# Performance work log

Hardware: AMD Instinct MI355X
Metric: run time of the kernel (lower is better)

## Reference

```python
import jax, jax.numpy as jnp
import numpy as np

L, C, H = 12, 1024, 16  # n_layer, n_embd, n_head
D = C // H
EPS = 1e-5

def gelu_new(x):
    # GPT-2 tanh-approximate GELU
    return 0.5 * x * (1.0 + jnp.tanh(np.sqrt(2.0 / np.pi).astype(np.float32) * (x + 0.044715 * x ** 3)))

def layernorm(x, g, b):
    mu = jnp.mean(x, axis=-1, keepdims=True)
    var = jnp.mean(jnp.square(x - mu), axis=-1, keepdims=True)
    return (x - mu) * jax.lax.rsqrt(var + EPS) * g + b

def setup_inputs() -> dict:
    key = jax.random.key(0)
    ks = jax.random.split(key, 8)
    std = 0.02
    inp = {
        'inputs_embeds': jax.random.normal(ks[0], (1, 1024, C), jnp.float32),
        'attention_mask': jnp.ones((1, 1024), jnp.float32),
        'ln1_g': jnp.ones((L, C), jnp.float32), 'ln1_b': jnp.zeros((L, C), jnp.float32),
        'Wqkv': jax.random.normal(ks[1], (L, C, 3 * C), jnp.float32) * std,
        'bqkv': jnp.zeros((L, 3 * C), jnp.float32),
        'Wo': jax.random.normal(ks[2], (L, C, C), jnp.float32) * (std / np.sqrt(2 * L)),
        'bo': jnp.zeros((L, C), jnp.float32),
        'ln2_g': jnp.ones((L, C), jnp.float32), 'ln2_b': jnp.zeros((L, C), jnp.float32),
        'Wfc': jax.random.normal(ks[3], (L, C, 4 * C), jnp.float32) * std,
        'bfc': jnp.zeros((L, 4 * C), jnp.float32),
        'Wmp': jax.random.normal(ks[4], (L, 4 * C, C), jnp.float32) * (std / np.sqrt(2 * L)),
        'bmp': jnp.zeros((L, C), jnp.float32),
        'lnf_g': jnp.ones((C,), jnp.float32), 'lnf_b': jnp.zeros((C,), jnp.float32),
    }
    return inp

def reference(inputs_embeds, attention_mask, ln1_g, ln1_b, Wqkv, bqkv, Wo, bo,
              ln2_g, ln2_b, Wfc, bfc, Wmp, bmp, lnf_g, lnf_b):
    B, T, _ = inputs_embeds.shape
    # padding mask -> additive bias [B,1,1,T] (broadcasts over heads and query dim)
    mask_add = -1e9 * (1.0 - attention_mask)[:, None, None, :]
    scale = 1.0 / np.sqrt(D).astype(np.float32)

    def block(x, p):
        g1, b1, Wq, bq, Wo_, bo_, g2, b2, Wf, bf, Wm, bm = p
        h = layernorm(x, g1, b1)
        qkv = h @ Wq + bq                                  # [B,T,3C]
        q, k, v = jnp.split(qkv, 3, axis=-1)
        q = q.reshape(B, T, H, D).transpose(0, 2, 1, 3)    # [B,H,T,D]
        k = k.reshape(B, T, H, D).transpose(0, 2, 1, 3)
        v = v.reshape(B, T, H, D).transpose(0, 2, 1, 3)
        att = jnp.einsum('bhqd,bhkd->bhqk', q, k) * scale + mask_add
        att = jax.nn.softmax(att, axis=-1)
        y = jnp.einsum('bhqk,bhkd->bhqd', att, v)
        y = y.transpose(0, 2, 1, 3).reshape(B, T, C)
        x = x + (y @ Wo_ + bo_)
        h2 = layernorm(x, g2, b2)
        x = x + (gelu_new(h2 @ Wf + bf) @ Wm + bm)
        return x, None

    params = (ln1_g, ln1_b, Wqkv, bqkv, Wo, bo, ln2_g, ln2_b, Wfc, bfc, Wmp, bmp)
    x, _ = jax.lax.scan(block, inputs_embeds, params)
    return layernorm(x, lnf_g, lnf_b)
```

## Files before the change

### kernel.cpp

```cpp
#include <hip/hip_runtime.h>
#include <hip/hip_bf16.h>
#include <math.h>

#define LN_EPS 1e-5f

typedef unsigned short u16;
typedef __attribute__((ext_vector_type(8))) _Float16 f16x8;
typedef __attribute__((ext_vector_type(4))) float f32x4;

__device__ __forceinline__ u16 f2h(float x) {
    _Float16 h = (_Float16)x;
    return __builtin_bit_cast(u16, h);
}
__device__ __forceinline__ void stv(float* p, float v) { *p = v; }
__device__ __forceinline__ void stv(u16* p, float v) { *p = f2h(v); }
__device__ __forceinline__ void stv4(float* p, float a, float b, float c, float d) {
    *(float4*)p = make_float4(a, b, c, d);
}
__device__ __forceinline__ void stv4(u16* p, float a, float b, float c, float d) {
    ushort4 o; o.x = f2h(a); o.y = f2h(b); o.z = f2h(c); o.w = f2h(d);
    *(ushort4*)p = o;
}

__device__ __forceinline__ float gelu_f(float x) {
    const float kA = 0.7978845608028654f;
    return 0.5f * x * (1.f + tanhf(kA * (x + 0.044715f * x * x * x)));
}

__device__ __forceinline__ void gl_lds16(const u16* g, u16* l) {
    __builtin_amdgcn_global_load_lds(
        (const __attribute__((address_space(1))) unsigned int*)g,
        (__attribute__((address_space(3))) unsigned int*)l, 16, 0, 0);
}
template <int N> __device__ __forceinline__ void s_vmcnt() {
    asm volatile("s_waitcnt vmcnt(%0)" :: "n"(N) : "memory");
}
__device__ __forceinline__ void s_lgkm0() {
    asm volatile("s_waitcnt lgkmcnt(0)" ::: "memory");
    __builtin_amdgcn_sched_barrier(0);
}
__device__ __forceinline__ void bar() { __builtin_amdgcn_s_barrier(); }
__device__ __forceinline__ void sfence() { __builtin_amdgcn_sched_barrier(0); }

__device__ __forceinline__ void cvt_tile(int t, const float* __restrict__ Wqkv,
                                         const float* __restrict__ Wo,
                                         const float* __restrict__ Wfc,
                                         const float* __restrict__ Wmp,
                                         u16* __restrict__ dst, float (*tile)[65]) {
    const float* W; u16* Wt; int K, N, idx;
    if (t < 768)       { W = Wqkv; Wt = dst;           K = 1024; N = 3072; idx = t; }
    else if (t < 1024) { W = Wo;   Wt = dst + 3145728; K = 1024; N = 1024; idx = t - 768; }
    else if (t < 2048) { W = Wfc;  Wt = dst + 4194304; K = 1024; N = 4096; idx = t - 1024; }
    else               { W = Wmp;  Wt = dst + 8388608; K = 4096; N = 1024; idx = t - 2048; }
    int ntn = N >> 6;
    int n0 = (idx % ntn) * 64, k0 = (idx / ntn) * 64;
    int th = threadIdx.x;
    int r = th >> 4, c4 = (th & 15) * 4;
#pragma unroll
    for (int p = 0; p < 4; p++) {
        float4 v = *(const float4*)(W + (size_t)(k0 + p * 16 + r) * N + n0 + c4);
        tile[p * 16 + r][c4 + 0] = v.x;
        tile[p * 16 + r][c4 + 1] = v.y;
        tile[p * 16 + r][c4 + 2] = v.z;
        tile[p * 16 + r][c4 + 3] = v.w;
    }
    __syncthreads();
#pragma unroll
    for (int p = 0; p < 4; p++) {
        int n = p * 16 + r;
        ushort4 o;
        o.x = f2h(tile[c4 + 0][n]);
        o.y = f2h(tile[c4 + 1][n]);
        o.z = f2h(tile[c4 + 2][n]);
        o.w = f2h(tile[c4 + 3][n]);
        *(ushort4*)(Wt + (size_t)(n0 + n) * K + k0 + c4) = o;
    }
}

__global__ __launch_bounds__(256) void tr_cvt_all(
    const float* __restrict__ Wqkv, const float* __restrict__ Wo,
    const float* __restrict__ Wfc, const float* __restrict__ Wmp,
    u16* __restrict__ dst) {
    __shared__ float tile[64][65];
    cvt_tile(blockIdx.x, Wqkv, Wo, Wfc, Wmp, dst, tile);
}

template <int PART, typename OT>
__global__ __launch_bounds__(256) void ln_cvt(float* __restrict__ x,
                                              const float* __restrict__ p0,
                                              const float* __restrict__ p1,
                                              const float* __restrict__ gam,
                                              const float* __restrict__ bet,
                                              OT* __restrict__ out,
                                              const float* __restrict__ cWq,
                                              const float* __restrict__ cWo,
                                              const float* __restrict__ cWf,
                                              const float* __restrict__ cWm,
                                              u16* __restrict__ cdst, int cbase) {
    __shared__ float tile[64][65];
    if (blockIdx.x >= 256) {
        cvt_tile(blockIdx.x - 256 + cbase, cWq, cWo, cWf, cWm, cdst, tile);
        return;
    }
    int w = threadIdx.x >> 6, lane = threadIdx.x & 63;
    int row = blockIdx.x * 4 + w;
    size_t base = (size_t)row * 1024;
    float4 v[4];
    float s = 0.f, ss = 0.f;
#pragma unroll
    for (int j = 0; j < 4; j++) {
        int c = lane * 4 + j * 256;
        float4 xv = *(const float4*)(x + base + c);
        if (PART) {
            float4 a = *(const float4*)(p0 + base + c);
            float4 b = *(const float4*)(p1 + base + c);
            xv.x += a.x + b.x; xv.y += a.y + b.y;
            xv.z += a.z + b.z; xv.w += a.w + b.w;
            *(float4*)(x + base + c) = xv;
        }
        v[j] = xv;
        s += xv.x + xv.y + xv.z + xv.w;
        ss += xv.x * xv.x + xv.y * xv.y + xv.z * xv.z + xv.w * xv.w;
    }
#pragma unroll
    for (int off = 32; off > 0; off >>= 1) {
        s += __shfl_xor(s, off);
        ss += __shfl_xor(ss, off);
    }
    float mu = s * (1.f / 1024.f);
    float var = ss * (1.f / 1024.f) - mu * mu;
    float rstd = rsqrtf(var + LN_EPS);
#pragma unroll
    for (int j = 0; j < 4; j++) {
        int c = lane * 4 + j * 256;
        float4 gv = *(const float4*)(gam + c);
        float4 bv = *(const float4*)(bet + c);
        stv4(&out[base + c],
             (v[j].x - mu) * rstd * gv.x + bv.x,
             (v[j].y - mu) * rstd * gv.y + bv.y,
             (v[j].z - mu) * rstd * gv.z + bv.z,
             (v[j].w - mu) * rstd * gv.w + bv.w);
    }
}

template <int BM, int BN, int BK, int WROW, int WCOL, int ACT, int WVT, int SPLITK,
          typename OT>
__global__ __launch_bounds__(WROW * WCOL * 64) void gemm_f16(
    const u16* __restrict__ A, const u16* __restrict__ Bt,
    const float* __restrict__ bias, OT* __restrict__ out,
    u16* __restrict__ vTout, int M, int N, int K) {
    __shared__ u16 As[2][BM * BK];
    __shared__ u16 Bs[2][BN * BK];
    constexpr int THREADS = WROW * WCOL * 64;
    constexpr int WM = BM / WROW, WN = BN / WCOL;
    constexpr int FM = WM / 16, FN = WN / 16;
    constexpr int NKF = BK / 32;
    constexpr int SLOTS = BK / 8;
    constexpr int ACH = BM * BK / 8 / THREADS;
    constexpr int BCH = BN * BK / 8 / THREADS;
    constexpr int LPS = ACH + BCH;
    int tid = threadIdx.x;
    int w = tid >> 6, l = tid & 63;
    int wm = w / WCOL, wn = w % WCOL;
    int lr = l & 15, g = l >> 4;
    int m0 = blockIdx.y * BM, n0 = blockIdx.x * BN;
    int kbase = (SPLITK > 1) ? blockIdx.z * (K / SPLITK) : 0;
    int Kc = (SPLITK > 1) ? (K / SPLITK) : K;
    OT* outz = (SPLITK > 1) ? out + (size_t)blockIdx.z * M * N : out;

    f32x4 acc[FM][FN] = {};

    auto stage = [&](int buf, int k0) {
#pragma unroll
        for (int i = 0; i < ACH; i++) {
            int chunk = i * THREADS + tid;
            int row = chunk / SLOTS, s = chunk % SLOTS, sg = s ^ (row & 7);
            gl_lds16(A + (size_t)(m0 + row) * K + kbase + k0 + sg * 8, &As[buf][chunk * 8]);
        }
#pragma unroll
        for (int i = 0; i < BCH; i++) {
            int chunk = i * THREADS + tid;
            int row = chunk / SLOTS, s = chunk % SLOTS, sg = s ^ (row & 7);
            gl_lds16(Bt + (size_t)(n0 + row) * K + kbase + k0 + sg * 8, &Bs[buf][chunk * 8]);
        }
    };

    int NT = Kc / BK;
    stage(0, 0);
    int cur = 0;
    for (int t = 0; t < NT; t++) {
        if (t + 1 < NT) { stage(cur ^ 1, (t + 1) * BK); s_vmcnt<LPS>(); }
        else            { s_vmcnt<0>(); }
        bar();
        sfence();

        const u16* Ab = &As[cur][0];
        const u16* Bb = &Bs[cur][0];
        f16x8 af[FM][NKF], bfrag[FN][NKF];
#pragma unroll
        for (int m = 0; m < FM; m++)
#pragma unroll
            for (int kf = 0; kf < NKF; kf++) {
                int row = wm * WM + m * 16 + lr;
                af[m][kf] = *(const f16x8*)(Ab + row * BK + (((kf * 4 + g) ^ (row & 7)) * 8));
            }
#pragma unroll
        for (int n = 0; n < FN; n++)
#pragma unroll
            for (int kf = 0; kf < NKF; kf++) {
                int row = wn * WN + n * 16 + lr;
                bfrag[n][kf] = *(const f16x8*)(Bb + row * BK + (((kf * 4 + g) ^ (row & 7)) * 8));
            }
#pragma unroll
        for (int kf = 0; kf < NKF; kf++)
#pragma unroll
            for (int m = 0; m < FM; m++)
#pragma unroll
                for (int n = 0; n < FN; n++)
                    acc[m][n] = __builtin_amdgcn_mfma_f32_16x16x32_f16(
                        af[m][kf], bfrag[n][kf], acc[m][n], 0, 0, 0);

        sfence();
        bar();
        cur ^= 1;
    }

#pragma unroll
    for (int m = 0; m < FM; m++) {
#pragma unroll
        for (int n = 0; n < FN; n++) {
            int col = n0 + wn * WN + n * 16 + lr;
            int row0 = m0 + wm * WM + m * 16 + 4 * g;
            float bv = (SPLITK > 1 && blockIdx.z != 0) ? 0.f : bias[col];
            u16 hv[4];
#pragma unroll
            for (int r = 0; r < 4; r++) {
                float v = acc[m][n][r] + bv;
                if (ACT) v = gelu_f(v);
                stv(&outz[(size_t)(row0 + r) * N + col], v);
                if (WVT) hv[r] = f2h(v);
            }
            if (WVT && col >= 2048) {
                ushort4 pv; pv.x = hv[0]; pv.y = hv[1]; pv.z = hv[2]; pv.w = hv[3];
                *(ushort4*)(vTout + (size_t)(col - 2048) * 1024 + row0) = pv;
            }
        }
    }
}

__global__ __launch_bounds__(256) void attn_mfma(
    const u16* __restrict__ qkv, const u16* __restrict__ vT,
    const float* __restrict__ mask, u16* __restrict__ y) {
    int h = blockIdx.y;
    int q0 = blockIdx.x * 64;
    int tid = threadIdx.x;
    int w = tid >> 6, l = tid & 63;
    int lr = l & 15, g = l >> 4;

    __shared__ u16 Ks[2][128 * 64];
    __shared__ u16 Vs[2][64 * 128];
    __shared__ u16 Ps[4 * 16 * 128];
    __shared__ float maskb[1024];

    for (int i = tid; i < 1024; i += 256) maskb[i] = -1e9f * (1.f - mask[i]);
    s_lgkm0();

    f16x8 qf[2];
#pragma unroll
    for (int kf = 0; kf < 2; kf++)
        qf[kf] = *(const f16x8*)(qkv + (size_t)(q0 + w * 16 + lr) * 3072 + h * 64 + kf * 32 + g * 8);

    f32x4 o[4] = {};
    float mrow[4], lrow[4];
#pragma unroll
    for (int r = 0; r < 4; r++) { mrow[r] = -1e30f; lrow[r] = 0.f; }

    u16* Psw = Ps + w * 2048;

    auto stage = [&](int buf, int kc) {
#pragma unroll
        for (int i = 0; i < 4; i++) {
            int chunk = i * 256 + tid;
            int krow = chunk >> 3, ks = chunk & 7, ksg = ks ^ (krow & 7);
            gl_lds16(qkv + (size_t)(kc * 128 + krow) * 3072 + 1024 + h * 64 + ksg * 8,
                     &Ks[buf][chunk * 8]);
            int vrow = chunk >> 4, vs = chunk & 15, vsg = vs ^ (vrow & 7);
            gl_lds16(vT + (size_t)(h * 64 + vrow) * 1024 + kc * 128 + vsg * 8,
                     &Vs[buf][chunk * 8]);
        }
    };

    stage(0, 0);
    int cur = 0;
    for (int kc = 0; kc < 8; kc++) {
        if (kc + 1 < 8) { stage(cur ^ 1, kc + 1); s_vmcnt<8>(); }
        else            { s_vmcnt<0>(); }
        bar();
        sfence();
        const u16* Kb = &Ks[cur][0];
        const u16* Vb = &Vs[cur][0];

        f32x4 s[8] = {};
        __builtin_amdgcn_s_setprio(1);
#pragma unroll
        for (int n = 0; n < 8; n++)
#pragma unroll
            for (int kf = 0; kf < 2; kf++) {
                int row = n * 16 + lr;
                f16x8 kfrag = *(const f16x8*)(Kb + row * 64 + (((kf * 4 + g) ^ (row & 7)) * 8));
                s[n] = __builtin_amdgcn_mfma_f32_16x16x32_f16(qf[kf], kfrag, s[n], 0, 0, 0);
            }
        __builtin_amdgcn_s_setprio(0);

        float mcol[8];
#pragma unroll
        for (int n = 0; n < 8; n++) mcol[n] = maskb[kc * 128 + n * 16 + lr];

        float scl[4], mnew[4], psum[4];
#pragma unroll
        for (int r = 0; r < 4; r++) {
            float mx = -1e30f;
#pragma unroll
            for (int n = 0; n < 8; n++) {
                float sv = s[n][r] * 0.125f + mcol[n];
                s[n][r] = sv;
                mx = fmaxf(mx, sv);
            }
            mx = fmaxf(mx, __shfl_xor(mx, 1));
            mx = fmaxf(mx, __shfl_xor(mx, 2));
            mx = fmaxf(mx, __shfl_xor(mx, 4));
            mx = fmaxf(mx, __shfl_xor(mx, 8));
            mnew[r] = fmaxf(mrow[r], mx);
            scl[r] = __expf(mrow[r] - mnew[r]);
            mrow[r] = mnew[r];
            psum[r] = 0.f;
        }
#pragma unroll
        for (int n = 0; n < 8; n++) {
            float p0 = __expf(s[n][0] - mnew[0]);
            float p1 = __expf(s[n][1] - mnew[1]);
            float p2 = __expf(s[n][2] - mnew[2]);
            float p3 = __expf(s[n][3] - mnew[3]);
            psum[0] += p0; psum[1] += p1; psum[2] += p2; psum[3] += p3;
            int col = n * 16 + lr, cs = col >> 3, cl = col & 7;
            int r0 = 4 * g;
            Psw[(r0 + 0) * 128 + ((cs ^ ((r0 + 0) & 7)) * 8) + cl] = f2h(p0);
            Psw[(r0 + 1) * 128 + ((cs ^ ((r0 + 1) & 7)) * 8) + cl] = f2h(p1);
            Psw[(r0 + 2) * 128 + ((cs ^ ((r0 + 2) & 7)) * 8) + cl] = f2h(p2);
            Psw[(r0 + 3) * 128 + ((cs ^ ((r0 + 3) & 7)) * 8) + cl] = f2h(p3);
        }
#pragma unroll
        for (int r = 0; r < 4; r++) {
            float ps_ = psum[r];
            ps_ += __shfl_xor(ps_, 1);
            ps_ += __shfl_xor(ps_, 2);
            ps_ += __shfl_xor(ps_, 4);
            ps_ += __shfl_xor(ps_, 8);
            lrow[r] = lrow[r] * scl[r] + ps_;
#pragma unroll
            for (int dn = 0; dn < 4; dn++) o[dn][r] *= scl[r];
        }

        f16x8 pa[4];
#pragma unroll
        for (int kf = 0; kf < 4; kf++)
            pa[kf] = *(const f16x8*)(Psw + lr * 128 + (((kf * 4 + g) ^ (lr & 7)) * 8));
        __builtin_amdgcn_s_setprio(1);
#pragma unroll
        for (int dn = 0; dn < 4; dn++) {
#pragma unroll
            for (int kf = 0; kf < 4; kf++) {
                int row = dn * 16 + lr;
                f16x8 vb = *(const f16x8*)(Vb + row * 128 + (((kf * 4 + g) ^ (row & 7)) * 8));
                o[dn] = __builtin_amdgcn_mfma_f32_16x16x32_f16(pa[kf], vb, o[dn], 0, 0, 0);
            }
        }
        __builtin_amdgcn_s_setprio(0);

        sfence();
        bar();
        cur ^= 1;
    }

    float inv[4];
#pragma unroll
    for (int r = 0; r < 4; r++) inv[r] = 1.f / lrow[r];
#pragma unroll
    for (int dn = 0; dn < 4; dn++)
#pragma unroll
        for (int r = 0; r < 4; r++) {
            int row = q0 + w * 16 + 4 * g + r;
            int col = h * 64 + dn * 16 + lr;
            y[(size_t)row * 1024 + col] = f2h(o[dn][r] * inv[r]);
        }
}

extern "C" void kernel_launch(void* const* d_in, const int* in_sizes, int n_in,
                              void* d_out, int out_size, void* d_ws, size_t ws_size,
                              hipStream_t stream) {
    const float* inputs_embeds = (const float*)d_in[0];
    const float* attn_mask     = (const float*)d_in[1];
    const float* ln1_g = (const float*)d_in[2];
    const float* ln1_b = (const float*)d_in[3];
    const float* Wqkv  = (const float*)d_in[4];
    const float* bqkv  = (const float*)d_in[5];
    const float* Wo    = (const float*)d_in[6];
    const float* bo    = (const float*)d_in[7];
    const float* ln2_g = (const float*)d_in[8];
    const float* ln2_b = (const float*)d_in[9];
    const float* Wfc   = (const float*)d_in[10];
    const float* bfc   = (const float*)d_in[11];
    const float* Wmp   = (const float*)d_in[12];
    const float* bmp   = (const float*)d_in[13];
    const float* lnf_g = (const float*)d_in[14];
    const float* lnf_b = (const float*)d_in[15];
    float* out = (float*)d_out;

    char* ws = (char*)d_ws;
    float* x   = (float*)ws;
    u16* hbuf  = (u16*)(ws + (4u << 20));
    u16* qkvb  = (u16*)(ws + (6u << 20));
    u16* fcb   = qkvb;
    u16* ybuf  = hbuf;
    u16* vTb   = (u16*)(ws + (14u << 20));
    u16* wbuf0 = (u16*)(ws + (16u << 20));
    u16* wbuf1 = (u16*)(ws + (40u << 20));
    float* pP  = (float*)(ws + (64u << 20));
    float* pM  = (float*)(ws + (72u << 20));

    hipMemcpyAsync(x, inputs_embeds, (size_t)(1 << 20) * sizeof(float),
                   hipMemcpyDeviceToDevice, stream);

    tr_cvt_all<<<3072, 256, 0, stream>>>(Wqkv, Wo, Wfc, Wmp, wbuf0);

    for (int l = 0; l < 12; l++) {
        u16* wb = (l & 1) ? wbuf1 : wbuf0;
        u16* wq = wb, *wo_ = wb + 3145728, *wf = wb + 4194304, *wm = wb + 8388608;

        bool cv = (l + 1 < 12);
        u16* nb = ((l + 1) & 1) ? wbuf1 : wbuf0;
        const float* nWq = cv ? Wqkv + (size_t)(l + 1) * 3145728 : nullptr;
        const float* nWo = cv ? Wo   + (size_t)(l + 1) * 1048576 : nullptr;
        const float* nWf = cv ? Wfc  + (size_t)(l + 1) * 4194304 : nullptr;
        const float* nWm = cv ? Wmp  + (size_t)(l + 1) * 4194304 : nullptr;
        int grid_ln = cv ? 256 + 1536 : 256;

        if (l == 0)
            ln_cvt<0, u16><<<grid_ln, 256, 0, stream>>>(
                x, nullptr, nullptr, ln1_g + l * 1024, ln1_b + l * 1024, hbuf,
                nWq, nWo, nWf, nWm, nb, 0);
        else
            ln_cvt<1, u16><<<grid_ln, 256, 0, stream>>>(
                x, pM, pM + (1 << 20), ln1_g + l * 1024, ln1_b + l * 1024, hbuf,
                nWq, nWo, nWf, nWm, nb, 0);

        gemm_f16<64, 128, 64, 2, 4, 0, 1, 1, u16><<<dim3(24, 16), 512, 0, stream>>>(
            hbuf, wq, bqkv + (size_t)l * 3072, qkvb, vTb, 1024, 3072, 1024);
        attn_mfma<<<dim3(16, 16), 256, 0, stream>>>(qkvb, vTb, attn_mask, ybuf);
        gemm_f16<64, 64, 128, 2, 2, 0, 0, 2, float><<<dim3(16, 16, 2), 256, 0, stream>>>(
            ybuf, wo_, bo + (size_t)l * 1024, pP, nullptr, 1024, 1024, 1024);
        ln_cvt<1, u16><<<grid_ln, 256, 0, stream>>>(
            x, pP, pP + (1 << 20), ln2_g + l * 1024, ln2_b + l * 1024, hbuf,
            nWq, nWo, nWf, nWm, nb, 1536);
        gemm_f16<128, 128, 64, 2, 4, 1, 0, 1, u16><<<dim3(32, 8), 512, 0, stream>>>(
            hbuf, wf, bfc + (size_t)l * 4096, fcb, nullptr, 1024, 4096, 1024);
        gemm_f16<64, 64, 128, 2, 2, 0, 0, 2, float><<<dim3(16, 16, 2), 256, 0, stream>>>(
            fcb, wm, bmp + (size_t)l * 1024, pM, nullptr, 1024, 1024, 4096);
    }
    ln_cvt<1, float><<<256, 256, 0, stream>>>(
        x, pM, pM + (1 << 20), lnf_g, lnf_b, out,
        nullptr, nullptr, nullptr, nullptr, nullptr, 0);
}
```

Measured before the change: 1.334 ms.

## Split attention over key halves with merge kernel; raise MLP-proj split-K to four

Attention now runs with a second grid dimension that splits the 1024 keys into two halves. Each half writes unnormalized fp32 partial outputs plus per-row max and sum, and a new merge kernel combines them with log-sum-exp rescaling into fp16 y. This doubles the attention block count from 256 to 512 so more compute units are busy. The MLP down-projection split-K goes from 2 to 4 partials, and the layernorm kernel now sums a generic number of partials. The cost is extra fp32 partial traffic, an extra kernel launch per layer, and more reads in the residual-add layernorm.

```diff
diff --git a/kernel.cpp b/kernel.cpp
--- a/kernel.cpp
+++ b/kernel.cpp
@@ -85,10 +85,9 @@
     cvt_tile(blockIdx.x, Wqkv, Wo, Wfc, Wmp, dst, tile);
 }
 
-template <int PART, typename OT>
+template <int PARTS, typename OT>
 __global__ __launch_bounds__(256) void ln_cvt(float* __restrict__ x,
-                                              const float* __restrict__ p0,
-                                              const float* __restrict__ p1,
+                                              const float* __restrict__ p,
                                               const float* __restrict__ gam,
                                               const float* __restrict__ bet,
                                               OT* __restrict__ out,
@@ -111,11 +110,12 @@
     for (int j = 0; j < 4; j++) {
         int c = lane * 4 + j * 256;
         float4 xv = *(const float4*)(x + base + c);
-        if (PART) {
-            float4 a = *(const float4*)(p0 + base + c);
-            float4 b = *(const float4*)(p1 + base + c);
-            xv.x += a.x + b.x; xv.y += a.y + b.y;
-            xv.z += a.z + b.z; xv.w += a.w + b.w;
+        if (PARTS) {
+#pragma unroll
+            for (int i = 0; i < PARTS; i++) {
+                float4 a = *(const float4*)(p + (size_t)i * (1u << 20) + base + c);
+                xv.x += a.x; xv.y += a.y; xv.z += a.z; xv.w += a.w;
+            }
             *(float4*)(x + base + c) = xv;
         }
         v[j] = xv;
@@ -250,9 +250,11 @@
 
 __global__ __launch_bounds__(256) void attn_mfma(
     const u16* __restrict__ qkv, const u16* __restrict__ vT,
-    const float* __restrict__ mask, u16* __restrict__ y) {
+    const float* __restrict__ mask, float* __restrict__ po,
+    float2* __restrict__ mlb) {
     int h = blockIdx.y;
     int q0 = blockIdx.x * 64;
+    int bz = blockIdx.z;
     int tid = threadIdx.x;
     int w = tid >> 6, l = tid & 63;
     int lr = l & 15, g = l >> 4;
@@ -290,11 +292,12 @@
         }
     };
 
-    stage(0, 0);
+    stage(0, bz * 4);
     int cur = 0;
-    for (int kc = 0; kc < 8; kc++) {
-        if (kc + 1 < 8) { stage(cur ^ 1, kc + 1); s_vmcnt<8>(); }
-        else            { s_vmcnt<0>(); }
+    for (int kcl = 0; kcl < 4; kcl++) {
+        int kc = bz * 4 + kcl;
+        if (kcl + 1 < 4) { stage(cur ^ 1, kc + 1); s_vmcnt<8>(); }
+        else             { s_vmcnt<0>(); }
         bar();
         sfence();
         const u16* Kb = &Ks[cur][0];
@@ -382,17 +385,47 @@
         cur ^= 1;
     }
 
-    float inv[4];
-#pragma unroll
-    for (int r = 0; r < 4; r++) inv[r] = 1.f / lrow[r];
+    float* poz = po + (size_t)bz * (1u << 20);
 #pragma unroll
     for (int dn = 0; dn < 4; dn++)
 #pragma unroll
         for (int r = 0; r < 4; r++) {
             int row = q0 + w * 16 + 4 * g + r;
             int col = h * 64 + dn * 16 + lr;
-            y[(size_t)row * 1024 + col] = f2h(o[dn][r] * inv[r]);
-        }
+            poz[(size_t)row * 1024 + col] = o[dn][r];
+        }
+    if (lr == 0) {
+#pragma unroll
+        for (int r = 0; r < 4; r++) {
+            int row = q0 + w * 16 + 4 * g + r;
+            mlb[bz * 16384 + row * 16 + h] = make_float2(mrow[r], lrow[r]);
+        }
+    }
+}
+
+__global__ __launch_bounds__(256) void attn_merge(const float* __restrict__ po,
+                                                  const float2* __restrict__ mlb,
+                                                  u16* __restrict__ y) {
+    int w = threadIdx.x >> 6, lane = threadIdx.x & 63;
+    int row = blockIdx.x * 4 + w;
+    size_t base = (size_t)row * 1024;
+#pragma unroll
+    for (int j = 0; j < 4; j++) {
+        int c = lane * 4 + j * 256;
+        int h = c >> 6;
+        float2 a = mlb[row * 16 + h];
+        float2 b = mlb[16384 + row * 16 + h];
+        float m = fmaxf(a.x, b.x);
+        float w0 = __expf(a.x - m), w1 = __expf(b.x - m);
+        float inv = 1.f / (w0 * a.y + w1 * b.y);
+        float4 o0 = *(const float4*)(po + base + c);
+        float4 o1 = *(const float4*)(po + (1u << 20) + base + c);
+        stv4(&y[base + c],
+             (w0 * o0.x + w1 * o1.x) * inv,
+             (w0 * o0.y + w1 * o1.y) * inv,
+             (w0 * o0.z + w1 * o1.z) * inv,
+             (w0 * o0.w + w1 * o1.w) * inv);
+    }
 }
 
 extern "C" void kernel_launch(void* const* d_in, const int* in_sizes, int n_in,
@@ -427,6 +460,8 @@
     u16* wbuf1 = (u16*)(ws + (40u << 20));
     float* pP  = (float*)(ws + (64u << 20));
     float* pM  = (float*)(ws + (72u << 20));
+    float* po  = (float*)(ws + (88u << 20));
+    float2* ml = (float2*)(ws + (96u << 20));
 
     hipMemcpyAsync(x, inputs_embeds, (size_t)(1 << 20) * sizeof(float),
                    hipMemcpyDeviceToDevice, stream);
@@ -447,27 +482,28 @@
 
         if (l == 0)
             ln_cvt<0, u16><<<grid_ln, 256, 0, stream>>>(
-                x, nullptr, nullptr, ln1_g + l * 1024, ln1_b + l * 1024, hbuf,
+                x, nullptr, ln1_g + l * 1024, ln1_b + l * 1024, hbuf,
                 nWq, nWo, nWf, nWm, nb, 0);
         else
-            ln_cvt<1, u16><<<grid_ln, 256, 0, stream>>>(
-                x, pM, pM + (1 << 20), ln1_g + l * 1024, ln1_b + l * 1024, hbuf,
+            ln_cvt<4, u16><<<grid_ln, 256, 0, stream>>>(
+                x, pM, ln1_g + l * 1024, ln1_b + l * 1024, hbuf,
                 nWq, nWo, nWf, nWm, nb, 0);
 
         gemm_f16<64, 128, 64, 2, 4, 0, 1, 1, u16><<<dim3(24, 16), 512, 0, stream>>>(
             hbuf, wq, bqkv + (size_t)l * 3072, qkvb, vTb, 1024, 3072, 1024);
-        attn_mfma<<<dim3(16, 16), 256, 0, stream>>>(qkvb, vTb, attn_mask, ybuf);
+        attn_mfma<<<dim3(16, 16, 2), 256, 0, stream>>>(qkvb, vTb, attn_mask, po, ml);
+        attn_merge<<<256, 256, 0, stream>>>(po, ml, ybuf);
         gemm_f16<64, 64, 128, 2, 2, 0, 0, 2, float><<<dim3(16, 16, 2), 256, 0, stream>>>(
             ybuf, wo_, bo + (size_t)l * 1024, pP, nullptr, 1024, 1024, 1024);
-        ln_cvt<1, u16><<<grid_ln, 256, 0, stream>>>(
-            x, pP, pP + (1 << 20), ln2_g + l * 1024, ln2_b + l * 1024, hbuf,
+        ln_cvt<2, u16><<<grid_ln, 256, 0, stream>>>(
+            x, pP, ln2_g + l * 1024, ln2_b + l * 1024, hbuf,
             nWq, nWo, nWf, nWm, nb, 1536);
         gemm_f16<128, 128, 64, 2, 4, 1, 0, 1, u16><<<dim3(32, 8), 512, 0, stream>>>(
             hbuf, wf, bfc + (size_t)l * 4096, fcb, nullptr, 1024, 4096, 1024);
-        gemm_f16<64, 64, 128, 2, 2, 0, 0, 2, float><<<dim3(16, 16, 2), 256, 0, stream>>>(
+        gemm_f16<64, 64, 128, 2, 2, 0, 0, 4, float><<<dim3(16, 16, 4), 256, 0, stream>>>(
             fcb, wm, bmp + (size_t)l * 1024, pM, nullptr, 1024, 1024, 4096);
     }
-    ln_cvt<1, float><<<256, 256, 0, stream>>>(
-        x, pM, pM + (1 << 20), lnf_g, lnf_b, out,
+    ln_cvt<4, float><<<256, 256, 0, stream>>>(
+        x, pM, lnf_g, lnf_b, out,
         nullptr, nullptr, nullptr, nullptr, nullptr, 0);
 }
```

Result: slower. 1.448 ms (+8.6%).
